# Kernel optimization log

Hardware: AMD Instinct MI355X
Metric: run time of the kernel (lower is better)

The kernel has to match this reference:

```python
import jax, jax.numpy as jnp
import numpy as np

B, T, H = 4, 4096, 1024


def setup_inputs() -> dict:
    key = jax.random.key(0)
    ks = jax.random.split(key, 10)
    W_STD = 0.02  # small init keeps the WKV denominator well-conditioned
    inp = {
        "x": jax.random.normal(ks[0], (B, T, H), dtype=jnp.float32),
        "time_decay": jnp.exp(-jax.random.uniform(ks[1], (H,), minval=0.5, maxval=1.5)),
        "time_mix_key": jax.random.uniform(ks[2], (H,)),
        "time_mix_value": jax.random.uniform(ks[3], (H,)),
        "time_mix_receptance": jax.random.uniform(ks[4], (H,)),
        "W_receptance": jax.random.normal(ks[5], (H, H)) * W_STD,
        "W_key": jax.random.normal(ks[6], (H, H)) * W_STD,
        "W_value": jax.random.normal(ks[7], (H, H)) * W_STD,
        "W_out": jax.random.normal(ks[8], (H, H)) * W_STD,
        "b_out": jax.random.normal(ks[9], (H,)) * W_STD,
    }
    return inp


def reference(x, time_decay, time_mix_key, time_mix_value, time_mix_receptance,
              W_receptance, W_key, W_value, W_out, b_out):
    # time_shift: shifted[:, t] = x[:, t-1], shifted[:, 0] = 0
    shifted = jnp.pad(x, ((0, 0), (1, 0), (0, 0)))[:, :-1]
    xs = x + shifted  # original applies SAME mix to x and shifted
    k = (xs * time_mix_key) @ W_key.T          # [B,T,H]
    v = (xs * time_mix_value) @ W_value.T      # [B,T,H]
    r = jax.nn.sigmoid((xs * time_mix_receptance) @ W_receptance.T)

    def step(carry, kv):
        num, den = carry                       # [B,H] each
        ck, cv = kv                            # [B,H]
        out = (num + time_decay * ck * den) / (den + time_decay * ck)
        ek = jnp.exp(ck)
        return (time_decay * num + ek * cv, time_decay * den + ek), out

    init = (jnp.ones_like(k[:, 0]), jnp.ones_like(k[:, 0]))
    kT = jnp.swapaxes(k, 0, 1)  # [T,B,H]
    vT = jnp.swapaxes(v, 0, 1)
    _, outT = jax.lax.scan(step, init, (kT, vT))
    out = jnp.swapaxes(outT, 0, 1)             # [B,T,H]
    return (r * out) @ W_out.T + b_out
```

## Files before the change

### kernel.cpp

```cpp
#include <hip/hip_runtime.h>

#define H_DIM 1024
#define T_DIM 4096
#define B_DIM 4
#define M_DIM (B_DIM * T_DIM)
#define SCAN_C 64
#define SCAN_W 48

typedef __attribute__((ext_vector_type(8))) short short8;
typedef __attribute__((ext_vector_type(4))) float f32x4;
typedef _Float16 half8 __attribute__((ext_vector_type(8)));

__device__ __forceinline__ unsigned short f2h(float f) {
  _Float16 h = (_Float16)f;
  return __builtin_bit_cast(unsigned short, h);
}
__device__ __forceinline__ float h2f(unsigned short u) {
  return (float)__builtin_bit_cast(_Float16, u);
}

__device__ __forceinline__ double fast_exp64(double x) {
  const double L2E = 1.4426950408889634074;
  const double LN2 = 0.69314718055994530942;
  double z = x * L2E;
  double n = rint(z);
  double y = (z - n) * LN2;
  double p = 2.7557319223985890653e-6;
  p = fma(p, y, 2.4801587301587301566e-5);
  p = fma(p, y, 1.9841269841269841253e-4);
  p = fma(p, y, 1.3888888888888889419e-3);
  p = fma(p, y, 8.3333333333333332177e-3);
  p = fma(p, y, 4.1666666666666664354e-2);
  p = fma(p, y, 1.6666666666666665741e-1);
  p = fma(p, y, 0.5);
  p = fma(p, y, 1.0);
  p = fma(p, y, 1.0);
  long long bits = ((long long)(1023 + (int)n)) << 52;
  return p * __longlong_as_double(bits);
}

__global__ void prep_kernel(const float* __restrict__ x,
                            const float* __restrict__ Wrec, const float* __restrict__ Wkey,
                            const float* __restrict__ Wval, const float* __restrict__ Wout,
                            const float* __restrict__ tmk, const float* __restrict__ tmv,
                            const float* __restrict__ tmr,
                            unsigned short* __restrict__ xs1, unsigned short* __restrict__ xs2,
                            unsigned short* __restrict__ WK1H, unsigned short* __restrict__ WK2H,
                            unsigned short* __restrict__ WVRH, unsigned short* __restrict__ WOH) {
  int bid = blockIdx.x;
  if (bid < 16384) {
    int i = bid * 256 + threadIdx.x;
    const int HV = H_DIM / 4;
    int m = i / HV;
    int t = m & (T_DIM - 1);
    float4 cur = reinterpret_cast<const float4*>(x)[i];
    float4 prev = make_float4(0.f, 0.f, 0.f, 0.f);
    if (t > 0) prev = reinterpret_cast<const float4*>(x)[i - HV];
    float s[4] = {cur.x + prev.x, cur.y + prev.y, cur.z + prev.z, cur.w + prev.w};
    unsigned short a1[4], a2[4];
#pragma unroll
    for (int q = 0; q < 4; ++q) {
      unsigned short h1 = f2h(s[q]);
      a1[q] = h1;
      a2[q] = f2h((s[q] - h2f(h1)) * 2048.0f);
    }
    reinterpret_cast<ushort4*>(xs1)[i] = make_ushort4(a1[0], a1[1], a1[2], a1[3]);
    reinterpret_cast<ushort4*>(xs2)[i] = make_ushort4(a2[0], a2[1], a2[2], a2[3]);
  } else {
    int i = (bid - 16384) * 256 + threadIdx.x;
    int j = i & (H_DIM - 1);
    float wk = Wkey[i] * tmk[j];
    unsigned short k1 = f2h(wk);
    WK1H[i] = k1;
    WK2H[i] = f2h((wk - h2f(k1)) * 2048.0f);
    WVRH[i] = f2h(Wval[i] * tmv[j]);
    WVRH[H_DIM * H_DIM + i] = f2h(Wrec[i] * tmr[j]);
    WOH[i] = f2h(Wout[i]);
  }
}

#define GBAR() do { asm volatile("" ::: "memory"); __builtin_amdgcn_sched_barrier(0); \
                    __builtin_amdgcn_s_barrier(); \
                    __builtin_amdgcn_sched_barrier(0); asm volatile("" ::: "memory"); } while (0)
#define WAIT_VM6() asm volatile("s_waitcnt vmcnt(6)" ::: "memory")
#define WAIT_VM0() asm volatile("s_waitcnt vmcnt(0)" ::: "memory")

__device__ __forceinline__ f32x4 mma_h(short8 a, short8 b, f32x4 c) {
  return __builtin_amdgcn_mfma_f32_16x16x32_f16(
      __builtin_bit_cast(half8, a), __builtin_bit_cast(half8, b), c, 0, 0, 0);
}

__device__ __forceinline__ void stage_r128(const unsigned short* base, int rowoff, int kt,
                                           unsigned dst, int wid, int lane,
                                           unsigned char* smem) {
  int row = wid * 16 + (lane >> 2);
  int col8 = (lane & 3) ^ ((row >> 1) & 3);
  const unsigned short* src = base + (size_t)(rowoff + row) * 1024 + kt * 32 + col8 * 8;
  __builtin_amdgcn_global_load_lds(
      (const __attribute__((address_space(1))) void*)src,
      (__attribute__((address_space(3))) void*)(smem + dst + wid * 1024), 16, 0, 0);
}
__device__ __forceinline__ void stage_r256(const unsigned short* base, int rowoff, int kt,
                                           unsigned dst, int wid, int lane,
                                           unsigned char* smem) {
#pragma unroll
  for (int i = 0; i < 2; ++i) {
    int row = wid * 32 + i * 16 + (lane >> 2);
    int col8 = (lane & 3) ^ ((row >> 1) & 3);
    const unsigned short* src = base + (size_t)(rowoff + row) * 1024 + kt * 32 + col8 * 8;
    __builtin_amdgcn_global_load_lds(
        (const __attribute__((address_space(1))) void*)src,
        (__attribute__((address_space(3))) void*)(smem + dst + wid * 2048 + i * 1024), 16, 0, 0);
  }
}
__device__ __forceinline__ short8 frag_ld2(const unsigned char* smem, unsigned rbase,
                                           int row, int kg) {
  return *reinterpret_cast<const short8*>(smem + rbase + row * 64 + ((kg ^ ((row >> 1) & 3)) * 16));
}

__device__ void gemm_k_body(const unsigned short* __restrict__ A1,
                            const unsigned short* __restrict__ A2,
                            const unsigned short* __restrict__ B1,
                            const unsigned short* __restrict__ B2,
                            float* __restrict__ C, int bid, unsigned char* smem) {
  const int tid = threadIdx.x;
  const int wid = tid >> 6;
  const int lane = tid & 63;
  const int wm = wid >> 2;
  const int wn = wid & 3;
  const int frow = lane & 15;
  const int kg = lane >> 4;
  const int swz = (bid & 7) * 64 + (bid >> 3);
  const int brow = (swz >> 2) << 7;
  const int bcol = (swz & 3) << 8;

  f32x4 acc0[4][4], acc1[4][4];
#pragma unroll
  for (int f = 0; f < 4; ++f)
#pragma unroll
    for (int c = 0; c < 4; ++c) {
      acc0[f][c] = (f32x4){0.f, 0.f, 0.f, 0.f};
      acc1[f][c] = (f32x4){0.f, 0.f, 0.f, 0.f};
    }

  const int NT = 32;
#pragma unroll
  for (int t0 = 0; t0 < 2; ++t0) {
    unsigned sb = t0 * 49152u;
    stage_r128(A1, brow, t0, sb + 0u, wid, lane, smem);
    stage_r128(A2, brow, t0, sb + 8192u, wid, lane, smem);
    stage_r256(B1, bcol, t0, sb + 16384u, wid, lane, smem);
    stage_r256(B2, bcol, t0, sb + 32768u, wid, lane, smem);
  }
  WAIT_VM6();
  GBAR();

  for (int t = 0; t < NT; ++t) {
    unsigned sb = (unsigned)(t % 3) * 49152u;
    unsigned st = (unsigned)((t + 2) % 3) * 49152u;
    const bool stg = (t + 2 < NT);
    short8 a1[4], a2[4], b1[4], b2[4];
#pragma unroll
    for (int f = 0; f < 4; ++f) a1[f] = frag_ld2(smem, sb + 0u, wm * 64 + f * 16 + frow, kg);
#pragma unroll
    for (int c = 0; c < 4; ++c) b1[c] = frag_ld2(smem, sb + 16384u, wn * 64 + c * 16 + frow, kg);
#pragma unroll
    for (int c = 0; c < 4; ++c) b2[c] = frag_ld2(smem, sb + 32768u, wn * 64 + c * 16 + frow, kg);
    if (stg) {
      stage_r128(A1, brow, t + 2, st + 0u, wid, lane, smem);
      stage_r128(A2, brow, t + 2, st + 8192u, wid, lane, smem);
    }
    GBAR();
    __builtin_amdgcn_s_setprio(1);
#pragma unroll
    for (int f = 0; f < 4; ++f)
#pragma unroll
      for (int c = 0; c < 4; ++c)
        acc0[f][c] = mma_h(a1[f], b1[c], acc0[f][c]);
#pragma unroll
    for (int f = 0; f < 4; ++f)
#pragma unroll
      for (int c = 0; c < 4; ++c)
        acc1[f][c] = mma_h(a1[f], b2[c], acc1[f][c]);
    __builtin_amdgcn_s_setprio(0);
    GBAR();
#pragma unroll
    for (int f = 0; f < 4; ++f) a2[f] = frag_ld2(smem, sb + 8192u, wm * 64 + f * 16 + frow, kg);
    if (stg) {
      stage_r256(B1, bcol, t + 2, st + 16384u, wid, lane, smem);
      stage_r256(B2, bcol, t + 2, st + 32768u, wid, lane, smem);
    }
    WAIT_VM6();
    GBAR();
    __builtin_amdgcn_s_setprio(1);
#pragma unroll
    for (int f = 0; f < 4; ++f)
#pragma unroll
      for (int c = 0; c < 4; ++c)
        acc1[f][c] = mma_h(a2[f], b1[c], acc1[f][c]);
    __builtin_amdgcn_s_setprio(0);
    GBAR();
  }
  WAIT_VM0();

#pragma unroll
  for (int f = 0; f < 4; ++f) {
    int r0 = brow + wm * 64 + f * 16 + kg * 4;
#pragma unroll
    for (int c = 0; c < 4; ++c) {
      int cc = bcol + wn * 64 + c * 16 + frow;
#pragma unroll
      for (int q = 0; q < 4; ++q)
        C[(size_t)(r0 + q) * H_DIM + cc] =
            fmaf(0.00048828125f, acc1[f][c][q], acc0[f][c][q]);
    }
  }
}

__device__ __forceinline__ void stage_half(const unsigned short* base, int rowoff,
                                           int ktp, int kk, int slot,
                                           int wid, int lane, unsigned char* smem) {
#pragma unroll
  for (int i = 0; i < 2; ++i) {
    int row = wid * 32 + i * 16 + (lane >> 2);
    int kcol8 = (lane & 3) ^ ((row >> 1) & 3);
    const unsigned short* src = base + (size_t)(rowoff + row) * 1024
                                + ktp * 64 + kk * 32 + kcol8 * 8;
    unsigned int doff = (unsigned int)(slot * 16384 + wid * 2048 + i * 1024);
    __builtin_amdgcn_global_load_lds(
        (const __attribute__((address_space(1))) void*)src,
        (__attribute__((address_space(3))) void*)(smem + doff), 16, 0, 0);
  }
}
__device__ __forceinline__ short8 frag_ld(const unsigned char* smem, int slot, int row, int kg) {
  int byte = slot * 16384 + row * 64 + ((kg ^ ((row >> 1) & 3)) * 16);
  return *reinterpret_cast<const short8*>(smem + byte);
}

__device__ void gemm_vr_body(const unsigned short* __restrict__ Ag,
                             const unsigned short* __restrict__ Bg,
                             unsigned short* __restrict__ C, int bid,
                             unsigned char* smem) {
  const int tid = threadIdx.x;
  const int wid = tid >> 6;
  const int lane = tid & 63;
  const int wm = wid >> 2;
  const int wn = wid & 3;
  const int frow = lane & 15;
  const int kg = lane >> 4;
  const int swz = (bid & 7) * 64 + (bid >> 3);
  const int brow = (swz >> 3) << 8;
  const int bcol = (swz & 7) << 8;

  f32x4 acc[8][4];
#pragma unroll
  for (int f = 0; f < 8; ++f)
#pragma unroll
    for (int c = 0; c < 4; ++c)
      acc[f][c] = (f32x4){0.f, 0.f, 0.f, 0.f};

  const int NT = 16;
  stage_half(Ag, brow, 0, 0, 0, wid, lane, smem);
  stage_half(Bg, bcol, 0, 0, 1, wid, lane, smem);
  stage_half(Ag, brow, 0, 1, 2, wid, lane, smem);
  stage_half(Bg, bcol, 0, 1, 3, wid, lane, smem);
  stage_half(Ag, brow, 1, 0, 4, wid, lane, smem);
  stage_half(Bg, bcol, 1, 0, 5, wid, lane, smem);
  stage_half(Ag, brow, 1, 1, 6, wid, lane, smem);
  WAIT_VM6();
  GBAR();

  for (int t = 0; t < NT; ++t) {
    const int cur4 = (t & 1) * 4;
    const int nxt4 = cur4 ^ 4;
    short8 a[4], b[4];
#pragma unroll
    for (int f = 0; f < 4; ++f) a[f] = frag_ld(smem, cur4 + 0, wm * 128 + f * 16 + frow, kg);
#pragma unroll
    for (int c = 0; c < 4; ++c) b[c] = frag_ld(smem, cur4 + 1, wn * 64 + c * 16 + frow, kg);
    if (t + 1 < NT) stage_half(Bg, bcol, t + 1, 1, nxt4 + 3, wid, lane, smem);
    GBAR();
    __builtin_amdgcn_s_setprio(1);
#pragma unroll
    for (int f = 0; f < 4; ++f)
#pragma unroll
      for (int c = 0; c < 4; ++c)
        acc[f][c] = mma_h(a[f], b[c], acc[f][c]);
    __builtin_amdgcn_s_setprio(0);
    GBAR();
#pragma unroll
    for (int f = 0; f < 4; ++f) a[f] = frag_ld(smem, cur4 + 0, wm * 128 + (f + 4) * 16 + frow, kg);
    if (t + 2 < NT) stage_half(Ag, brow, t + 2, 0, cur4 + 0, wid, lane, smem);
    GBAR();
    __builtin_amdgcn_s_setprio(1);
#pragma unroll
    for (int f = 0; f < 4; ++f)
#pragma unroll
      for (int c = 0; c < 4; ++c)
        acc[f + 4][c] = mma_h(a[f], b[c], acc[f + 4][c]);
    __builtin_amdgcn_s_setprio(0);
    GBAR();
#pragma unroll
    for (int f = 0; f < 4; ++f) a[f] = frag_ld(smem, cur4 + 2, wm * 128 + f * 16 + frow, kg);
#pragma unroll
    for (int c = 0; c < 4; ++c) b[c] = frag_ld(smem, cur4 + 3, wn * 64 + c * 16 + frow, kg);
    if (t + 2 < NT) stage_half(Bg, bcol, t + 2, 0, cur4 + 1, wid, lane, smem);
    GBAR();
    __builtin_amdgcn_s_setprio(1);
#pragma unroll
    for (int f = 0; f < 4; ++f)
#pragma unroll
      for (int c = 0; c < 4; ++c)
        acc[f][c] = mma_h(a[f], b[c], acc[f][c]);
    __builtin_amdgcn_s_setprio(0);
    GBAR();
#pragma unroll
    for (int f = 0; f < 4; ++f) a[f] = frag_ld(smem, cur4 + 2, wm * 128 + (f + 4) * 16 + frow, kg);
    if (t + 2 < NT) stage_half(Ag, brow, t + 2, 1, cur4 + 2, wid, lane, smem);
    WAIT_VM6();
    GBAR();
    __builtin_amdgcn_s_setprio(1);
#pragma unroll
    for (int f = 0; f < 4; ++f)
#pragma unroll
      for (int c = 0; c < 4; ++c)
        acc[f + 4][c] = mma_h(a[f], b[c], acc[f + 4][c]);
    __builtin_amdgcn_s_setprio(0);
    GBAR();
  }
  WAIT_VM0();

#pragma unroll
  for (int f = 0; f < 8; ++f) {
    int r0 = brow + wm * 128 + f * 16 + kg * 4;
#pragma unroll
    for (int c = 0; c < 4; ++c) {
      int cc = bcol + wn * 64 + c * 16 + frow;
#pragma unroll
      for (int q = 0; q < 4; ++q)
        C[(size_t)(r0 + q) * 2048 + cc] = f2h(acc[f][c][q]);
    }
  }
}

__global__ __launch_bounds__(512, 2) void front_kernel(
    const unsigned short* __restrict__ XS1, const unsigned short* __restrict__ XS2,
    const unsigned short* __restrict__ WK1, const unsigned short* __restrict__ WK2,
    const unsigned short* __restrict__ WVR,
    float* __restrict__ Ck, unsigned short* __restrict__ Cvr) {
  __shared__ __attribute__((aligned(16))) unsigned char smem[147456];
  int bid = blockIdx.x;
  if (bid < 512)
    gemm_k_body(XS1, XS2, WK1, WK2, Ck, bid, smem);
  else
    gemm_vr_body(XS1, WVR, Cvr, bid - 512, smem);
}

__global__ __launch_bounds__(512, 2) void gemm_o_kernel(const unsigned short* __restrict__ Ag,
                                                        const unsigned short* __restrict__ Bg,
                                                        float* __restrict__ C,
                                                        const float* __restrict__ bias) {
  __shared__ __attribute__((aligned(16))) unsigned char smem[131072];
  const int tid = threadIdx.x;
  const int wid = tid >> 6;
  const int lane = tid & 63;
  const int wm = wid >> 2;
  const int wn = wid & 3;
  const int frow = lane & 15;
  const int kg = lane >> 4;
  const int nwg = gridDim.x * gridDim.y;
  const int wg = blockIdx.y * gridDim.x + blockIdx.x;
  const int swz = (wg & 7) * (nwg >> 3) + (wg >> 3);
  const int brow = (swz / gridDim.x) << 8;
  const int bcol = (swz % gridDim.x) << 8;

  f32x4 acc[8][4];
#pragma unroll
  for (int f = 0; f < 8; ++f)
#pragma unroll
    for (int c = 0; c < 4; ++c)
      acc[f][c] = (f32x4){0.f, 0.f, 0.f, 0.f};

  const int NT = 16;
  stage_half(Ag, brow, 0, 0, 0, wid, lane, smem);
  stage_half(Bg, bcol, 0, 0, 1, wid, lane, smem);
  stage_half(Ag, brow, 0, 1, 2, wid, lane, smem);
  stage_half(Bg, bcol, 0, 1, 3, wid, lane, smem);
  stage_half(Ag, brow, 1, 0, 4, wid, lane, smem);
  stage_half(Bg, bcol, 1, 0, 5, wid, lane, smem);
  stage_half(Ag, brow, 1, 1, 6, wid, lane, smem);
  WAIT_VM6();
  GBAR();

  for (int t = 0; t < NT; ++t) {
    const int cur4 = (t & 1) * 4;
    const int nxt4 = cur4 ^ 4;
    short8 a[4], b[4];
#pragma unroll
    for (int f = 0; f < 4; ++f) a[f] = frag_ld(smem, cur4 + 0, wm * 128 + f * 16 + frow, kg);
#pragma unroll
    for (int c = 0; c < 4; ++c) b[c] = frag_ld(smem, cur4 + 1, wn * 64 + c * 16 + frow, kg);
    if (t + 1 < NT) stage_half(Bg, bcol, t + 1, 1, nxt4 + 3, wid, lane, smem);
    GBAR();
    __builtin_amdgcn_s_setprio(1);
#pragma unroll
    for (int f = 0; f < 4; ++f)
#pragma unroll
      for (int c = 0; c < 4; ++c)
        acc[f][c] = mma_h(a[f], b[c], acc[f][c]);
    __builtin_amdgcn_s_setprio(0);
    GBAR();
#pragma unroll
    for (int f = 0; f < 4; ++f) a[f] = frag_ld(smem, cur4 + 0, wm * 128 + (f + 4) * 16 + frow, kg);
    if (t + 2 < NT) stage_half(Ag, brow, t + 2, 0, cur4 + 0, wid, lane, smem);
    GBAR();
    __builtin_amdgcn_s_setprio(1);
#pragma unroll
    for (int f = 0; f < 4; ++f)
#pragma unroll
      for (int c = 0; c < 4; ++c)
        acc[f + 4][c] = mma_h(a[f], b[c], acc[f + 4][c]);
    __builtin_amdgcn_s_setprio(0);
    GBAR();
#pragma unroll
    for (int f = 0; f < 4; ++f) a[f] = frag_ld(smem, cur4 + 2, wm * 128 + f * 16 + frow, kg);
#pragma unroll
    for (int c = 0; c < 4; ++c) b[c] = frag_ld(smem, cur4 + 3, wn * 64 + c * 16 + frow, kg);
    if (t + 2 < NT) stage_half(Bg, bcol, t + 2, 0, cur4 + 1, wid, lane, smem);
    GBAR();
    __builtin_amdgcn_s_setprio(1);
#pragma unroll
    for (int f = 0; f < 4; ++f)
#pragma unroll
      for (int c = 0; c < 4; ++c)
        acc[f][c] = mma_h(a[f], b[c], acc[f][c]);
    __builtin_amdgcn_s_setprio(0);
    GBAR();
#pragma unroll
    for (int f = 0; f < 4; ++f) a[f] = frag_ld(smem, cur4 + 2, wm * 128 + (f + 4) * 16 + frow, kg);
    if (t + 2 < NT) stage_half(Ag, brow, t + 2, 1, cur4 + 2, wid, lane, smem);
    WAIT_VM6();
    GBAR();
    __builtin_amdgcn_s_setprio(1);
#pragma unroll
    for (int f = 0; f < 4; ++f)
#pragma unroll
      for (int c = 0; c < 4; ++c)
        acc[f + 4][c] = mma_h(a[f], b[c], acc[f + 4][c]);
    __builtin_amdgcn_s_setprio(0);
    GBAR();
  }
  WAIT_VM0();

#pragma unroll
  for (int f = 0; f < 8; ++f) {
    int r0 = brow + wm * 128 + f * 16 + kg * 4;
#pragma unroll
    for (int c = 0; c < 4; ++c) {
      int cc = bcol + wn * 64 + c * 16 + frow;
      float bb = bias[cc];
#pragma unroll
      for (int q = 0; q < 4; ++q)
        C[(size_t)(r0 + q) * H_DIM + cc] = acc[f][c][q] + bb;
    }
  }
}

__global__ void wkv_scan_kernel(const float* __restrict__ kbuf,
                                const unsigned short* __restrict__ vrbuf,
                                const float* __restrict__ tdec,
                                unsigned short* __restrict__ rwh) {
  const int h = (blockIdx.x * 64 + threadIdx.x) * 2;
  const int chunk = blockIdx.y;
  const int b = blockIdx.z;
  const int t0 = chunk * SCAN_C;
  const int tstart = (chunk == 0) ? 0 : (t0 - SCAN_W);
  const int tend = t0 + SCAN_C;
  double num0, den0, num1, den1;
  if (chunk == 0) { num0 = num1 = 1.0; den0 = den1 = 1.0; }
  else            { num0 = num1 = 0.0; den0 = den1 = 0.0; }
  const double w0 = (double)tdec[h];
  const double w1 = (double)tdec[h + 1];
  size_t ik = ((size_t)b * T_DIM + tstart) * H_DIM + h;
  size_t iv = ((size_t)b * T_DIM + tstart) * 2048 + h;
  float2 kc = *reinterpret_cast<const float2*>(kbuf + ik);
  unsigned int vc = *reinterpret_cast<const unsigned int*>(vrbuf + iv);
  unsigned int rc = *reinterpret_cast<const unsigned int*>(vrbuf + iv + 1024);
  for (int t = tstart; t < tend; ++t) {
    size_t adv = (t + 1 < tend) ? 1 : 0;
    float2 kn = *reinterpret_cast<const float2*>(kbuf + ik + adv * H_DIM);
    unsigned int vn = *reinterpret_cast<const unsigned int*>(vrbuf + iv + adv * 2048);
    unsigned int rn = *reinterpret_cast<const unsigned int*>(vrbuf + iv + adv * 2048 + 1024);
    double ck0 = (double)kc.x, ck1 = (double)kc.y;
    if (t >= t0) {
      double p0 = w0 * ck0, p1 = w1 * ck1;
      float o0 = (float)fma(p0, den0, num0) / (float)(den0 + p0);
      float o1 = (float)fma(p1, den1, num1) / (float)(den1 + p1);
      float rr0 = 1.0f / (1.0f + __expf(-h2f((unsigned short)(rc & 0xffffu))));
      float rr1 = 1.0f / (1.0f + __expf(-h2f((unsigned short)(rc >> 16))));
      unsigned int wout = (unsigned int)f2h(rr0 * o0) | ((unsigned int)f2h(rr1 * o1) << 16);
      *reinterpret_cast<unsigned int*>(rwh + ik) = wout;
    }
    double ek0 = fast_exp64(ck0);
    double ek1 = fast_exp64(ck1);
    num0 = fma(w0, num0, ek0 * (double)h2f((unsigned short)(vc & 0xffffu)));
    den0 = fma(w0, den0, ek0);
    num1 = fma(w1, num1, ek1 * (double)h2f((unsigned short)(vc >> 16)));
    den1 = fma(w1, den1, ek1);
    kc = kn; vc = vn; rc = rn;
    ik += H_DIM; iv += 2048;
  }
}

extern "C" void kernel_launch(void* const* d_in, const int* in_sizes, int n_in,
                              void* d_out, int out_size, void* d_ws, size_t ws_size,
                              hipStream_t stream) {
  const float* x    = (const float*)d_in[0];
  const float* tdec = (const float*)d_in[1];
  const float* tmk  = (const float*)d_in[2];
  const float* tmv  = (const float*)d_in[3];
  const float* tmr  = (const float*)d_in[4];
  const float* Wrec = (const float*)d_in[5];
  const float* Wkey = (const float*)d_in[6];
  const float* Wval = (const float*)d_in[7];
  const float* Wout = (const float*)d_in[8];
  const float* bout = (const float*)d_in[9];
  float* out = (float*)d_out;
  unsigned char* ws = (unsigned char*)d_ws;

  const size_t W2 = (size_t)H_DIM * H_DIM * 2;
  const size_t BF_FULL = (size_t)M_DIM * H_DIM * 2;
  const size_t NEED = 2 * BF_FULL + 2 * BF_FULL + 5 * W2;
  if (ws_size < NEED) return;

  size_t off = 0;
  unsigned short* XS1H = (unsigned short*)(ws + off); off += BF_FULL;
  unsigned short* XS2H = (unsigned short*)(ws + off); off += BF_FULL;
  unsigned short* VR   = (unsigned short*)(ws + off); off += 2 * BF_FULL;
  unsigned short* WK1H = (unsigned short*)(ws + off); off += W2;
  unsigned short* WK2H = (unsigned short*)(ws + off); off += W2;
  unsigned short* WVRH = (unsigned short*)(ws + off); off += 2 * W2;
  unsigned short* WOH  = (unsigned short*)(ws + off); off += W2;

  prep_kernel<<<dim3(16384 + 4096), dim3(256), 0, stream>>>(
      x, Wrec, Wkey, Wval, Wout, tmk, tmv, tmr, XS1H, XS2H, WK1H, WK2H, WVRH, WOH);

  front_kernel<<<dim3(1024), dim3(512), 0, stream>>>(
      XS1H, XS2H, WK1H, WK2H, WVRH, out, VR);

  unsigned short* RWH = XS1H;
  wkv_scan_kernel<<<dim3(H_DIM / 128, T_DIM / SCAN_C, B_DIM), dim3(64), 0, stream>>>(
      out, VR, tdec, RWH);

  gemm_o_kernel<<<dim3(H_DIM / 256, M_DIM / 256), dim3(512), 0, stream>>>(
      RWH, WOH, out, bout);
}
```

Measured before the change: 303.5 us.

## Shrink output GEMM tile, reorder k-GEMM fragment loads, halve scan chunk

The output projection GEMM moves from 256x256 tiles with 128 KB of LDS to 128x256 tiles with a three-stage 24 KB ring (72 KB), launched as 512 blocks with launch bounds raised to 4. The aim is more resident blocks and a finer swizzled grid in exchange for less reuse per tile. The k-GEMM in the front kernel now loads the B2 fragments later and moves the a1*B2 MFMAs into the second phase, lowering register pressure. Both GEMMs now drain with vmcnt(0) on the last iterations, and the WKV scan chunk shrinks from 64 to 32, giving more parallel blocks but a larger share of redundant warm-up steps.

Result: no change. 305.7 us (+0.7%).

```diff
diff --git a/kernel.cpp b/kernel.cpp
--- a/kernel.cpp
+++ b/kernel.cpp
@@ -4,7 +4,7 @@
 #define T_DIM 4096
 #define B_DIM 4
 #define M_DIM (B_DIM * T_DIM)
-#define SCAN_C 64
+#define SCAN_C 32
 #define SCAN_W 48
 
 typedef __attribute__((ext_vector_type(8))) short short8;
@@ -83,6 +83,7 @@
                     __builtin_amdgcn_s_barrier(); \
                     __builtin_amdgcn_sched_barrier(0); asm volatile("" ::: "memory"); } while (0)
 #define WAIT_VM6() asm volatile("s_waitcnt vmcnt(6)" ::: "memory")
+#define WAIT_VM3() asm volatile("s_waitcnt vmcnt(3)" ::: "memory")
 #define WAIT_VM0() asm volatile("s_waitcnt vmcnt(0)" ::: "memory")
 
 __device__ __forceinline__ f32x4 mma_h(short8 a, short8 b, f32x4 c) {
@@ -164,8 +165,6 @@
     for (int f = 0; f < 4; ++f) a1[f] = frag_ld2(smem, sb + 0u, wm * 64 + f * 16 + frow, kg);
 #pragma unroll
     for (int c = 0; c < 4; ++c) b1[c] = frag_ld2(smem, sb + 16384u, wn * 64 + c * 16 + frow, kg);
-#pragma unroll
-    for (int c = 0; c < 4; ++c) b2[c] = frag_ld2(smem, sb + 32768u, wn * 64 + c * 16 + frow, kg);
     if (stg) {
       stage_r128(A1, brow, t + 2, st + 0u, wid, lane, smem);
       stage_r128(A2, brow, t + 2, st + 8192u, wid, lane, smem);
@@ -177,22 +176,26 @@
 #pragma unroll
       for (int c = 0; c < 4; ++c)
         acc0[f][c] = mma_h(a1[f], b1[c], acc0[f][c]);
-#pragma unroll
-    for (int f = 0; f < 4; ++f)
-#pragma unroll
-      for (int c = 0; c < 4; ++c)
-        acc1[f][c] = mma_h(a1[f], b2[c], acc1[f][c]);
-    __builtin_amdgcn_s_setprio(0);
-    GBAR();
+    __builtin_amdgcn_s_setprio(0);
+    GBAR();
+#pragma unroll
+    for (int c = 0; c < 4; ++c) b2[c] = frag_ld2(smem, sb + 32768u, wn * 64 + c * 16 + frow, kg);
 #pragma unroll
     for (int f = 0; f < 4; ++f) a2[f] = frag_ld2(smem, sb + 8192u, wm * 64 + f * 16 + frow, kg);
     if (stg) {
       stage_r256(B1, bcol, t + 2, st + 16384u, wid, lane, smem);
       stage_r256(B2, bcol, t + 2, st + 32768u, wid, lane, smem);
-    }
-    WAIT_VM6();
-    GBAR();
-    __builtin_amdgcn_s_setprio(1);
+      WAIT_VM6();
+    } else {
+      WAIT_VM0();
+    }
+    GBAR();
+    __builtin_amdgcn_s_setprio(1);
+#pragma unroll
+    for (int f = 0; f < 4; ++f)
+#pragma unroll
+      for (int c = 0; c < 4; ++c)
+        acc1[f][c] = mma_h(a1[f], b2[c], acc1[f][c]);
 #pragma unroll
     for (int f = 0; f < 4; ++f)
 #pragma unroll
@@ -317,7 +320,7 @@
 #pragma unroll
     for (int f = 0; f < 4; ++f) a[f] = frag_ld(smem, cur4 + 2, wm * 128 + (f + 4) * 16 + frow, kg);
     if (t + 2 < NT) stage_half(Ag, brow, t + 2, 1, cur4 + 2, wid, lane, smem);
-    WAIT_VM6();
+    if (t + 2 < NT) { WAIT_VM6(); } else { WAIT_VM0(); }
     GBAR();
     __builtin_amdgcn_s_setprio(1);
 #pragma unroll
@@ -356,11 +359,11 @@
     gemm_vr_body(XS1, WVR, Cvr, bid - 512, smem);
 }
 
-__global__ __launch_bounds__(512, 2) void gemm_o_kernel(const unsigned short* __restrict__ Ag,
+__global__ __launch_bounds__(512, 4) void gemm_o_kernel(const unsigned short* __restrict__ Ag,
                                                         const unsigned short* __restrict__ Bg,
                                                         float* __restrict__ C,
                                                         const float* __restrict__ bias) {
-  __shared__ __attribute__((aligned(16))) unsigned char smem[131072];
+  __shared__ __attribute__((aligned(16))) unsigned char smem[73728];
   const int tid = threadIdx.x;
   const int wid = tid >> 6;
   const int lane = tid & 63;
@@ -368,39 +371,44 @@
   const int wn = wid & 3;
   const int frow = lane & 15;
   const int kg = lane >> 4;
-  const int nwg = gridDim.x * gridDim.y;
-  const int wg = blockIdx.y * gridDim.x + blockIdx.x;
-  const int swz = (wg & 7) * (nwg >> 3) + (wg >> 3);
-  const int brow = (swz / gridDim.x) << 8;
-  const int bcol = (swz % gridDim.x) << 8;
-
-  f32x4 acc[8][4];
-#pragma unroll
-  for (int f = 0; f < 8; ++f)
+  const int bid = blockIdx.x;
+  const int swz = (bid & 7) * 64 + (bid >> 3);
+  const int brow = (swz >> 2) << 7;
+  const int bcol = (swz & 3) << 8;
+
+  f32x4 acc[4][4];
+#pragma unroll
+  for (int f = 0; f < 4; ++f)
 #pragma unroll
     for (int c = 0; c < 4; ++c)
       acc[f][c] = (f32x4){0.f, 0.f, 0.f, 0.f};
 
-  const int NT = 16;
-  stage_half(Ag, brow, 0, 0, 0, wid, lane, smem);
-  stage_half(Bg, bcol, 0, 0, 1, wid, lane, smem);
-  stage_half(Ag, brow, 0, 1, 2, wid, lane, smem);
-  stage_half(Bg, bcol, 0, 1, 3, wid, lane, smem);
-  stage_half(Ag, brow, 1, 0, 4, wid, lane, smem);
-  stage_half(Bg, bcol, 1, 0, 5, wid, lane, smem);
-  stage_half(Ag, brow, 1, 1, 6, wid, lane, smem);
-  WAIT_VM6();
+  const int NT = 32;
+#pragma unroll
+  for (int t0 = 0; t0 < 2; ++t0) {
+    unsigned sb = t0 * 24576u;
+    stage_r128(Ag, brow, t0, sb + 0u, wid, lane, smem);
+    stage_r256(Bg, bcol, t0, sb + 8192u, wid, lane, smem);
+  }
+  WAIT_VM3();
   GBAR();
 
   for (int t = 0; t < NT; ++t) {
-    const int cur4 = (t & 1) * 4;
-    const int nxt4 = cur4 ^ 4;
+    unsigned sb = (unsigned)(t % 3) * 24576u;
+    unsigned st = (unsigned)((t + 2) % 3) * 24576u;
+    const bool stg = (t + 2 < NT);
     short8 a[4], b[4];
 #pragma unroll
-    for (int f = 0; f < 4; ++f) a[f] = frag_ld(smem, cur4 + 0, wm * 128 + f * 16 + frow, kg);
-#pragma unroll
-    for (int c = 0; c < 4; ++c) b[c] = frag_ld(smem, cur4 + 1, wn * 64 + c * 16 + frow, kg);
-    if (t + 1 < NT) stage_half(Bg, bcol, t + 1, 1, nxt4 + 3, wid, lane, smem);
+    for (int f = 0; f < 4; ++f) a[f] = frag_ld2(smem, sb + 0u, wm * 64 + f * 16 + frow, kg);
+#pragma unroll
+    for (int c = 0; c < 4; ++c) b[c] = frag_ld2(smem, sb + 8192u, wn * 64 + c * 16 + frow, kg);
+    if (stg) {
+      stage_r128(Ag, brow, t + 2, st + 0u, wid, lane, smem);
+      stage_r256(Bg, bcol, t + 2, st + 8192u, wid, lane, smem);
+      WAIT_VM3();
+    } else {
+      WAIT_VM0();
+    }
     GBAR();
     __builtin_amdgcn_s_setprio(1);
 #pragma unroll
@@ -410,51 +418,12 @@
         acc[f][c] = mma_h(a[f], b[c], acc[f][c]);
     __builtin_amdgcn_s_setprio(0);
     GBAR();
-#pragma unroll
-    for (int f = 0; f < 4; ++f) a[f] = frag_ld(smem, cur4 + 0, wm * 128 + (f + 4) * 16 + frow, kg);
-    if (t + 2 < NT) stage_half(Ag, brow, t + 2, 0, cur4 + 0, wid, lane, smem);
-    GBAR();
-    __builtin_amdgcn_s_setprio(1);
-#pragma unroll
-    for (int f = 0; f < 4; ++f)
-#pragma unroll
-      for (int c = 0; c < 4; ++c)
-        acc[f + 4][c] = mma_h(a[f], b[c], acc[f + 4][c]);
-    __builtin_amdgcn_s_setprio(0);
-    GBAR();
-#pragma unroll
-    for (int f = 0; f < 4; ++f) a[f] = frag_ld(smem, cur4 + 2, wm * 128 + f * 16 + frow, kg);
-#pragma unroll
-    for (int c = 0; c < 4; ++c) b[c] = frag_ld(smem, cur4 + 3, wn * 64 + c * 16 + frow, kg);
-    if (t + 2 < NT) stage_half(Bg, bcol, t + 2, 0, cur4 + 1, wid, lane, smem);
-    GBAR();
-    __builtin_amdgcn_s_setprio(1);
-#pragma unroll
-    for (int f = 0; f < 4; ++f)
-#pragma unroll
-      for (int c = 0; c < 4; ++c)
-        acc[f][c] = mma_h(a[f], b[c], acc[f][c]);
-    __builtin_amdgcn_s_setprio(0);
-    GBAR();
-#pragma unroll
-    for (int f = 0; f < 4; ++f) a[f] = frag_ld(smem, cur4 + 2, wm * 128 + (f + 4) * 16 + frow, kg);
-    if (t + 2 < NT) stage_half(Ag, brow, t + 2, 1, cur4 + 2, wid, lane, smem);
-    WAIT_VM6();
-    GBAR();
-    __builtin_amdgcn_s_setprio(1);
-#pragma unroll
-    for (int f = 0; f < 4; ++f)
-#pragma unroll
-      for (int c = 0; c < 4; ++c)
-        acc[f + 4][c] = mma_h(a[f], b[c], acc[f + 4][c]);
-    __builtin_amdgcn_s_setprio(0);
-    GBAR();
   }
   WAIT_VM0();
 
 #pragma unroll
-  for (int f = 0; f < 8; ++f) {
-    int r0 = brow + wm * 128 + f * 16 + kg * 4;
+  for (int f = 0; f < 4; ++f) {
+    int r0 = brow + wm * 64 + f * 16 + kg * 4;
 #pragma unroll
     for (int c = 0; c < 4; ++c) {
       int cc = bcol + wn * 64 + c * 16 + frow;
@@ -474,11 +443,12 @@
   const int chunk = blockIdx.y;
   const int b = blockIdx.z;
   const int t0 = chunk * SCAN_C;
-  const int tstart = (chunk == 0) ? 0 : (t0 - SCAN_W);
+  int tstart = t0 - SCAN_W;
+  if (tstart < 0) tstart = 0;
   const int tend = t0 + SCAN_C;
   double num0, den0, num1, den1;
-  if (chunk == 0) { num0 = num1 = 1.0; den0 = den1 = 1.0; }
-  else            { num0 = num1 = 0.0; den0 = den1 = 0.0; }
+  if (tstart == 0) { num0 = num1 = 1.0; den0 = den1 = 1.0; }
+  else             { num0 = num1 = 0.0; den0 = den1 = 0.0; }
   const double w0 = (double)tdec[h];
   const double w1 = (double)tdec[h + 1];
   size_t ik = ((size_t)b * T_DIM + tstart) * H_DIM + h;
@@ -552,6 +522,5 @@
   wkv_scan_kernel<<<dim3(H_DIM / 128, T_DIM / SCAN_C, B_DIM), dim3(64), 0, stream>>>(
       out, VR, tdec, RWH);
 
-  gemm_o_kernel<<<dim3(H_DIM / 256, M_DIM / 256), dim3(512), 0, stream>>>(
-      RWH, WOH, out, bout);
-}
+  gemm_o_kernel<<<dim3(512), dim3(512), 0, stream>>>(RWH, WOH, out, bout);
+}
```
